# Performance work log

Measured on AMD Instinct MI355X. Metric: run time of the kernel, lower is better.

The kernel has to match this reference:

```python
import jax, jax.numpy as jnp
import numpy as np

N_NODES = 100000
N_EDGES = 1600000
N_FEATS = 128
N_CLASSES = 40
K_HOPS = 3


def setup_inputs() -> dict:
    key = jax.random.key(0)
    k1, k2, k3, k4 = jax.random.split(key, 4)
    x = jax.random.normal(k1, (N_NODES, N_FEATS), dtype=jnp.float32)
    edge_index = jax.random.randint(k2, (2, N_EDGES), 0, N_NODES, dtype=jnp.int64)
    edge_weight = jax.random.uniform(k3, (N_EDGES,), dtype=jnp.float32)
    # Linear layer of SGConv (bias=False): [num_feats, num_classes]
    W = jax.random.normal(k4, (N_FEATS, N_CLASSES), dtype=jnp.float32) / np.sqrt(N_FEATS)
    return {"x": x, "edge_index": edge_index, "edge_weight": edge_weight, "W": W}


def reference(x, edge_index, edge_weight, W):
    # SGConv forward: gcn_norm (symmetric, no self-loops), K hops of
    # edge-weighted gather/scatter aggregation, then linear (lin_first=False).
    row, col = edge_index[0], edge_index[1]
    # symmetric normalization: deg from target-node scatter of edge weights
    deg = jax.ops.segment_sum(edge_weight, col, num_segments=N_NODES)
    deg_inv_sqrt = jnp.where(deg > 0, jax.lax.rsqrt(jnp.maximum(deg, 1e-30)), 0.0)
    norm = deg_inv_sqrt[row] * edge_weight * deg_inv_sqrt[col]  # [E]
    h = x
    for _ in range(K_HOPS):
        msgs = h[row] * norm[:, None]                 # [E, F] gather + scale
        h = jax.ops.segment_sum(msgs, col, num_segments=N_NODES)  # [N, F] scatter-add
    return h @ W  # [N, num_classes]
```

## Files before the change

### kernel.cpp

```cpp
#include <hip/hip_runtime.h>
#include <hip/hip_fp16.h>

namespace {
constexpr int NN = 100000;
constexpr int NE = 1600000;
constexpr int NF = 128;
constexpr int NC = 40;
constexpr int HP = 64;
constexpr int NB = (NN + 255) / 256;
constexpr int EB = (NE + 255) / 256;
constexpr float FIX = 1048576.0f;
constexpr int NPB = 51;
constexpr int HB  = (NN + NPB - 1) / NPB;
constexpr int TS  = 2048;
}

struct alignas(16) H8 { __half2 a, b, c, d; };

__device__ inline __half2 f2h2(float x, float y) {
    return __halves2half2(__float2half_rn(x), __float2half_rn(y));
}

__global__ __launch_bounds__(256, 2) void k_build(const int* __restrict__ col,
                                                  const float* __restrict__ w,
                                                  const float* __restrict__ x,
                                                  const float* __restrict__ W,
                                                  unsigned long long* __restrict__ dc,
                                                  unsigned char* __restrict__ rank,
                                                  __half* __restrict__ h0) {
    if (blockIdx.x < (unsigned)NB) {
        int n = blockIdx.x * 256 + threadIdx.x;
        if (n >= NN) return;
        const float4* xr = (const float4*)(x + (size_t)n * NF);
        const float4* W4 = (const float4*)W;
        float acc[NC];
#pragma unroll
        for (int j = 0; j < NC; ++j) acc[j] = 0.f;
        for (int k4 = 0; k4 < NF / 4; ++k4) {
            float4 xv = xr[k4];
#pragma unroll
            for (int kk = 0; kk < 4; ++kk) {
                float xk = (kk == 0) ? xv.x : (kk == 1) ? xv.y : (kk == 2) ? xv.z : xv.w;
                int k = k4 * 4 + kk;
#pragma unroll
                for (int j4 = 0; j4 < 10; ++j4) {
                    float4 wv = W4[k * 10 + j4];
                    acc[j4 * 4 + 0] += xk * wv.x;
                    acc[j4 * 4 + 1] += xk * wv.y;
                    acc[j4 * 4 + 2] += xk * wv.z;
                    acc[j4 * 4 + 3] += xk * wv.w;
                }
            }
        }
        H8* o = (H8*)(h0 + (size_t)n * HP);
#pragma unroll
        for (int g = 0; g < 5; ++g) {
            H8 v;
            v.a = f2h2(acc[g * 8 + 0], acc[g * 8 + 1]);
            v.b = f2h2(acc[g * 8 + 2], acc[g * 8 + 3]);
            v.c = f2h2(acc[g * 8 + 4], acc[g * 8 + 5]);
            v.d = f2h2(acc[g * 8 + 6], acc[g * 8 + 7]);
            o[g] = v;
        }
    } else {
        int e = (blockIdx.x - NB) * 256 + threadIdx.x;
        if (e >= NE) return;
        int c = col[e];
        unsigned long long q = (unsigned long long)(unsigned)(w[e] * FIX + 0.5f);
        unsigned long long old = atomicAdd(&dc[c], (1ull << 40) | q);
        rank[e] = (unsigned char)(old >> 40);
    }
}

__global__ __launch_bounds__(256) void k_scan1(const unsigned long long* __restrict__ dc,
                                               int* __restrict__ offs,
                                               int* __restrict__ bsum,
                                               float* __restrict__ dis) {
    __shared__ int s[256];
    int t = threadIdx.x, i = blockIdx.x * 256 + t;
    unsigned long long p = (i < NN) ? dc[i] : 0ull;
    int v = (int)(p >> 40);
    if (i < NN) {
        float d = (float)(p & ((1ull << 40) - 1)) * (1.0f / FIX);
        dis[i] = (d > 0.f) ? rsqrtf(d) : 0.f;
    }
    s[t] = v;
    __syncthreads();
    for (int off = 1; off < 256; off <<= 1) {
        int add = (t >= off) ? s[t - off] : 0;
        __syncthreads();
        s[t] += add;
        __syncthreads();
    }
    if (i < NN) offs[i] = s[t] - v;
    if (t == 255) bsum[blockIdx.x] = s[255];
}

__global__ __launch_bounds__(512) void k_scan2(int* __restrict__ bsum) {
    __shared__ int s[512];
    int t = threadIdx.x;
    int v = (t < NB) ? bsum[t] : 0;
    s[t] = v;
    __syncthreads();
    for (int off = 1; off < 512; off <<= 1) {
        int add = (t >= off) ? s[t - off] : 0;
        __syncthreads();
        s[t] += add;
        __syncthreads();
    }
    if (t < NB) bsum[t] = s[t] - v;
}

__global__ __launch_bounds__(256) void k_scatter(const int* __restrict__ row,
                                                 const int* __restrict__ col,
                                                 const float* __restrict__ w,
                                                 const float* __restrict__ dis,
                                                 const int* __restrict__ offs,
                                                 const int* __restrict__ bsum,
                                                 const unsigned char* __restrict__ rank,
                                                 int2* __restrict__ pair) {
    int e = blockIdx.x * 256 + threadIdx.x;
    if (e >= NE) return;
    int r = row[e], c = col[e];
    int p = offs[c] + bsum[c >> 8] + rank[e];
    unsigned long long v = (unsigned long long)(unsigned)r |
        ((unsigned long long)(unsigned)__float_as_int(dis[r] * w[e] * dis[c]) << 32);
    __builtin_nontemporal_store(v, (unsigned long long*)(pair + p));
}

template <bool FINAL>
__global__ __launch_bounds__(256) void k_hop(const int* __restrict__ offs,
                                             const int* __restrict__ bsum,
                                             const int2* __restrict__ pair,
                                             const __half* __restrict__ hin,
                                             __half* __restrict__ houth,
                                             float* __restrict__ houtf) {
    __shared__ int2 tile[TS];
    __shared__ int erange[2];
    int t = threadIdx.x;
    int g = t / 5;
    int n = blockIdx.x * NPB + g;
    bool active = (t < NPB * 5) && (n < NN);
    int vo = (t - g * 5) * 8;
    int s0 = 0, s1 = 0;
    if (active) {
        s0 = offs[n] + bsum[n >> 8];
        int np = n + 1;
        s1 = (np == NN) ? NE : (offs[np] + bsum[np >> 8]);
    }
    if (t == 0) {
        int n0 = blockIdx.x * NPB;
        erange[0] = offs[n0] + bsum[n0 >> 8];
        int nl = n0 + NPB;
        erange[1] = (nl >= NN) ? NE : (offs[nl] + bsum[nl >> 8]);
    }
    __syncthreads();
    int E0 = erange[0], E1 = erange[1];
    float acc[8];
#pragma unroll
    for (int j = 0; j < 8; ++j) acc[j] = 0.f;
    int i = s0;
    for (int t0 = E0; t0 < E1; t0 += TS) {
        int lim = min(t0 + TS, E1);
        int cnt = lim - t0;
        for (int j = t; j < cnt; j += 256) tile[j] = pair[t0 + j];
        __syncthreads();
        if (active) {
            int hi = min(s1, lim);
            for (; i + 2 <= hi; i += 2) {
                int2 p0 = tile[i - t0];
                int2 p1 = tile[i + 1 - t0];
                H8 m0 = *(const H8*)(hin + (size_t)p0.x * HP + vo);
                H8 m1 = *(const H8*)(hin + (size_t)p1.x * HP + vo);
                float w0 = __int_as_float(p0.y);
                float w1 = __int_as_float(p1.y);
                float2 f;
                f = __half22float2(m0.a); acc[0] += f.x * w0; acc[1] += f.y * w0;
                f = __half22float2(m0.b); acc[2] += f.x * w0; acc[3] += f.y * w0;
                f = __half22float2(m0.c); acc[4] += f.x * w0; acc[5] += f.y * w0;
                f = __half22float2(m0.d); acc[6] += f.x * w0; acc[7] += f.y * w0;
                f = __half22float2(m1.a); acc[0] += f.x * w1; acc[1] += f.y * w1;
                f = __half22float2(m1.b); acc[2] += f.x * w1; acc[3] += f.y * w1;
                f = __half22float2(m1.c); acc[4] += f.x * w1; acc[5] += f.y * w1;
                f = __half22float2(m1.d); acc[6] += f.x * w1; acc[7] += f.y * w1;
            }
            if (i < hi) {
                int2 p0 = tile[i - t0];
                H8 m0 = *(const H8*)(hin + (size_t)p0.x * HP + vo);
                float w0 = __int_as_float(p0.y);
                float2 f;
                f = __half22float2(m0.a); acc[0] += f.x * w0; acc[1] += f.y * w0;
                f = __half22float2(m0.b); acc[2] += f.x * w0; acc[3] += f.y * w0;
                f = __half22float2(m0.c); acc[4] += f.x * w0; acc[5] += f.y * w0;
                f = __half22float2(m0.d); acc[6] += f.x * w0; acc[7] += f.y * w0;
                ++i;
            }
        }
        __syncthreads();
    }
    if (active) {
        if (FINAL) {
            float* o = houtf + (size_t)n * NC + vo;
            float4 v0 = {acc[0], acc[1], acc[2], acc[3]};
            float4 v1 = {acc[4], acc[5], acc[6], acc[7]};
            *(float4*)(o) = v0;
            *(float4*)(o + 4) = v1;
        } else {
            H8 v;
            v.a = f2h2(acc[0], acc[1]);
            v.b = f2h2(acc[2], acc[3]);
            v.c = f2h2(acc[4], acc[5]);
            v.d = f2h2(acc[6], acc[7]);
            *(H8*)(houth + (size_t)n * HP + vo) = v;
        }
    }
}

extern "C" void kernel_launch(void* const* d_in, const int* in_sizes, int n_in,
                              void* d_out, int out_size, void* d_ws, size_t ws_size,
                              hipStream_t stream) {
    const float* x  = (const float*)d_in[0];
    const int*   ei = (const int*)d_in[1];
    const float* w  = (const float*)d_in[2];
    const float* W  = (const float*)d_in[3];
    const int* row = ei;
    const int* col = ei + NE;
    float* out = (float*)d_out;

    char* base = (char*)d_ws;
    __half* hb = (__half*)base;
    unsigned long long* dc = (unsigned long long*)base;
    float* dis = (float*)(base + (size_t)NN * 8);
    unsigned char* rank = (unsigned char*)(base + (size_t)NN * 12);
    char* p = base + (size_t)NN * HP * 2;
    int*  offs = (int*)p;   p += (size_t)(NN + 4) * 4;
    int*  bsum = (int*)p;   p += 512 * 4;
    int2* pair = (int2*)p;  p += (size_t)NE * 8;
    __half* ha = (__half*)p;

    hipMemsetAsync(dc, 0, (size_t)NN * 8, stream);
    k_build<<<NB + EB, 256, 0, stream>>>(col, w, x, W, dc, rank, ha);
    k_scan1<<<NB, 256, 0, stream>>>(dc, offs, bsum, dis);
    k_scan2<<<1, 512, 0, stream>>>(bsum);
    k_scatter<<<EB, 256, 0, stream>>>(row, col, w, dis, offs, bsum, rank, pair);

    k_hop<false><<<HB, 256, 0, stream>>>(offs, bsum, pair, ha, hb, nullptr);
    k_hop<false><<<HB, 256, 0, stream>>>(offs, bsum, pair, hb, ha, nullptr);
    k_hop<true ><<<HB, 256, 0, stream>>>(offs, bsum, pair, ha, nullptr, out);
}
```

Baseline: 328.8 us.

## Batch degree atomics per thread and fuse scan passes via last-block pattern

The degree/count atomic pass now handles eight edges per thread with loads hoisted ahead of the atomics, and those blocks are scheduled before the node projection blocks. The two scan kernels merge into one: the last block to finish, found with an atomic done counter and thread fences, performs the block-sum scan. This saves a kernel launch and gives the atomics more memory-level parallelism, at the cost of a serialized tail in the final block and an extra counter that must be zeroed.

```diff
diff --git a/kernel.cpp b/kernel.cpp
--- a/kernel.cpp
+++ b/kernel.cpp
@@ -9,6 +9,9 @@
 constexpr int HP = 64;
 constexpr int NB = (NN + 255) / 256;
 constexpr int EB = (NE + 255) / 256;
+constexpr int EPT = 8;
+constexpr int DB = 782;
+constexpr int DS = DB * 256;
 constexpr float FIX = 1048576.0f;
 constexpr int NPB = 51;
 constexpr int HB  = (NN + NPB - 1) / NPB;
@@ -28,8 +31,31 @@
                                                   unsigned long long* __restrict__ dc,
                                                   unsigned char* __restrict__ rank,
                                                   __half* __restrict__ h0) {
-    if (blockIdx.x < (unsigned)NB) {
-        int n = blockIdx.x * 256 + threadIdx.x;
+    if (blockIdx.x < (unsigned)DB) {
+        int base = blockIdx.x * 256 + threadIdx.x;
+        int cs[EPT];
+        float wv[EPT];
+        unsigned long long old[EPT];
+#pragma unroll
+        for (int k = 0; k < EPT; ++k) {
+            int e = base + k * DS;
+            if (e < NE) { cs[k] = col[e]; wv[k] = w[e]; }
+        }
+#pragma unroll
+        for (int k = 0; k < EPT; ++k) {
+            int e = base + k * DS;
+            if (e < NE) {
+                unsigned long long q = (unsigned long long)(unsigned)(wv[k] * FIX + 0.5f);
+                old[k] = atomicAdd(&dc[cs[k]], (1ull << 40) | q);
+            }
+        }
+#pragma unroll
+        for (int k = 0; k < EPT; ++k) {
+            int e = base + k * DS;
+            if (e < NE) rank[e] = (unsigned char)(old[k] >> 40);
+        }
+    } else {
+        int n = (blockIdx.x - DB) * 256 + threadIdx.x;
         if (n >= NN) return;
         const float4* xr = (const float4*)(x + (size_t)n * NF);
         const float4* W4 = (const float4*)W;
@@ -44,11 +70,11 @@
                 int k = k4 * 4 + kk;
 #pragma unroll
                 for (int j4 = 0; j4 < 10; ++j4) {
-                    float4 wv = W4[k * 10 + j4];
-                    acc[j4 * 4 + 0] += xk * wv.x;
-                    acc[j4 * 4 + 1] += xk * wv.y;
-                    acc[j4 * 4 + 2] += xk * wv.z;
-                    acc[j4 * 4 + 3] += xk * wv.w;
+                    float4 wq = W4[k * 10 + j4];
+                    acc[j4 * 4 + 0] += xk * wq.x;
+                    acc[j4 * 4 + 1] += xk * wq.y;
+                    acc[j4 * 4 + 2] += xk * wq.z;
+                    acc[j4 * 4 + 3] += xk * wq.w;
                 }
             }
         }
@@ -62,21 +88,16 @@
             v.d = f2h2(acc[g * 8 + 6], acc[g * 8 + 7]);
             o[g] = v;
         }
-    } else {
-        int e = (blockIdx.x - NB) * 256 + threadIdx.x;
-        if (e >= NE) return;
-        int c = col[e];
-        unsigned long long q = (unsigned long long)(unsigned)(w[e] * FIX + 0.5f);
-        unsigned long long old = atomicAdd(&dc[c], (1ull << 40) | q);
-        rank[e] = (unsigned char)(old >> 40);
-    }
-}
-
-__global__ __launch_bounds__(256) void k_scan1(const unsigned long long* __restrict__ dc,
-                                               int* __restrict__ offs,
-                                               int* __restrict__ bsum,
-                                               float* __restrict__ dis) {
+    }
+}
+
+__global__ __launch_bounds__(256) void k_scan(const unsigned long long* __restrict__ dc,
+                                              int* __restrict__ offs,
+                                              int* __restrict__ bsum,
+                                              float* __restrict__ dis,
+                                              int* __restrict__ done) {
     __shared__ int s[256];
+    __shared__ int amLast;
     int t = threadIdx.x, i = blockIdx.x * 256 + t;
     unsigned long long p = (i < NN) ? dc[i] : 0ull;
     int v = (int)(p >> 40);
@@ -94,21 +115,26 @@
     }
     if (i < NN) offs[i] = s[t] - v;
     if (t == 255) bsum[blockIdx.x] = s[255];
-}
-
-__global__ __launch_bounds__(512) void k_scan2(int* __restrict__ bsum) {
-    __shared__ int s[512];
-    int t = threadIdx.x;
-    int v = (t < NB) ? bsum[t] : 0;
-    s[t] = v;
-    __syncthreads();
+    __threadfence();
+    if (t == 0) amLast = (atomicAdd(done, 1) == NB - 1) ? 1 : 0;
+    __syncthreads();
+    if (!amLast) return;
+    __threadfence();
+    __shared__ int a[512], b[512];
+    int i0 = t, i1 = t + 256;
+    int v0 = (i0 < NB) ? bsum[i0] : 0;
+    int v1 = (i1 < NB) ? bsum[i1] : 0;
+    a[i0] = v0; a[i1] = v1;
+    __syncthreads();
+    int* cur = a; int* nxt = b;
     for (int off = 1; off < 512; off <<= 1) {
-        int add = (t >= off) ? s[t - off] : 0;
-        __syncthreads();
-        s[t] += add;
-        __syncthreads();
-    }
-    if (t < NB) bsum[t] = s[t] - v;
+        nxt[i0] = cur[i0] + ((i0 >= off) ? cur[i0 - off] : 0);
+        nxt[i1] = cur[i1] + ((i1 >= off) ? cur[i1 - off] : 0);
+        __syncthreads();
+        int* tmp = cur; cur = nxt; nxt = tmp;
+    }
+    if (i0 < NB) bsum[i0] = cur[i0] - v0;
+    if (i1 < NB) bsum[i1] = cur[i1] - v1;
 }
 
 __global__ __launch_bounds__(256) void k_scatter(const int* __restrict__ row,
@@ -230,18 +256,18 @@
     char* base = (char*)d_ws;
     __half* hb = (__half*)base;
     unsigned long long* dc = (unsigned long long*)base;
-    float* dis = (float*)(base + (size_t)NN * 8);
-    unsigned char* rank = (unsigned char*)(base + (size_t)NN * 12);
+    int* done = (int*)(base + (size_t)NN * 8);
+    float* dis = (float*)(base + (size_t)NN * 8 + 16);
+    unsigned char* rank = (unsigned char*)(base + (size_t)NN * 12 + 16);
     char* p = base + (size_t)NN * HP * 2;
     int*  offs = (int*)p;   p += (size_t)(NN + 4) * 4;
     int*  bsum = (int*)p;   p += 512 * 4;
     int2* pair = (int2*)p;  p += (size_t)NE * 8;
     __half* ha = (__half*)p;
 
-    hipMemsetAsync(dc, 0, (size_t)NN * 8, stream);
-    k_build<<<NB + EB, 256, 0, stream>>>(col, w, x, W, dc, rank, ha);
-    k_scan1<<<NB, 256, 0, stream>>>(dc, offs, bsum, dis);
-    k_scan2<<<1, 512, 0, stream>>>(bsum);
+    hipMemsetAsync(dc, 0, (size_t)NN * 8 + 16, stream);
+    k_build<<<DB + NB, 256, 0, stream>>>(col, w, x, W, dc, rank, ha);
+    k_scan<<<NB, 256, 0, stream>>>(dc, offs, bsum, dis, done);
     k_scatter<<<EB, 256, 0, stream>>>(row, col, w, dis, offs, bsum, rank, pair);
 
     k_hop<false><<<HB, 256, 0, stream>>>(offs, bsum, pair, ha, hb, nullptr);
```

Result: slower. 367.0 us (+11.6%).
